# Performance work log

Hardware: AMD Instinct MI355X
Metric: run time of the kernel (lower is better)

## Reference

```python
import jax, jax.numpy as jnp
import numpy as np

N, E, G = 30000, 480000, 64
IN, MID, HEADS, OUT = 256, (64, 64, 128), 8, 13


def _tconv(x, src, dst, ea, qw, qb, kw, kb, vw, vb, ew, sw, sb, heads, n):
    # PyG TransformerConv (concat=True, root_weight=True, beta=False), eval mode
    d = qw.shape[1] // heads
    q = (x @ qw + qb)[dst].reshape(-1, heads, d)   # [E,H,d] query at target
    k = (x @ kw + kb)[src].reshape(-1, heads, d)   # [E,H,d] key at source
    v = (x @ vw + vb)[src].reshape(-1, heads, d)   # [E,H,d] value at source
    e = (ea @ ew).reshape(-1, heads, d)            # [E,H,d] edge embedding (no bias)
    k = k + e
    a = (q * k).sum(-1) / jnp.sqrt(jnp.asarray(d, x.dtype))   # [E,H]
    amax = jax.ops.segment_max(a, dst, num_segments=n)        # segment softmax over in-edges
    ex = jnp.exp(a - amax[dst])
    den = jax.ops.segment_sum(ex, dst, num_segments=n)
    alpha = ex / den[dst]
    out = jax.ops.segment_sum((v + e) * alpha[..., None], dst, num_segments=n)
    out = out.reshape(n, heads * d)
    return out + x @ sw + sb                        # root/skip connection


def _mk(key, shape):
    return jax.random.normal(key, shape, dtype=jnp.float32) * 0.05


def setup_inputs() -> dict:
    key = jax.random.key(0)
    ks = iter(jax.random.split(key, 40))
    inp = {
        "x": jax.random.normal(next(ks), (N, IN), dtype=jnp.float32),
        "edge_index": jax.random.randint(next(ks), (2, E), 0, N, dtype=jnp.int64),
        "edge_attr": jax.random.normal(next(ks), (E, 1), dtype=jnp.float32),
        "batch": jnp.sort(jax.random.randint(next(ks), (N,), 0, G, dtype=jnp.int64)),
    }
    # conv1: in=256 -> heads=8, d=64 (out 512)
    o1 = HEADS * MID[0]
    inp.update(q1w=_mk(next(ks), (IN, o1)), q1b=_mk(next(ks), (o1,)),
               k1w=_mk(next(ks), (IN, o1)), k1b=_mk(next(ks), (o1,)),
               v1w=_mk(next(ks), (IN, o1)), v1b=_mk(next(ks), (o1,)),
               e1w=_mk(next(ks), (1, o1)),
               s1w=_mk(next(ks), (IN, o1)), s1b=_mk(next(ks), (o1,)))
    # conv2: in=512 -> heads=4, d=64 (out 256)
    h2, i2 = HEADS // 2, o1
    o2 = h2 * MID[1]
    inp.update(q2w=_mk(next(ks), (i2, o2)), q2b=_mk(next(ks), (o2,)),
               k2w=_mk(next(ks), (i2, o2)), k2b=_mk(next(ks), (o2,)),
               v2w=_mk(next(ks), (i2, o2)), v2b=_mk(next(ks), (o2,)),
               e2w=_mk(next(ks), (1, o2)),
               s2w=_mk(next(ks), (i2, o2)), s2b=_mk(next(ks), (o2,)))
    # conv3: in=256 -> heads=1, d=128
    i3, o3 = o2, MID[2]
    inp.update(q3w=_mk(next(ks), (i3, o3)), q3b=_mk(next(ks), (o3,)),
               k3w=_mk(next(ks), (i3, o3)), k3b=_mk(next(ks), (o3,)),
               v3w=_mk(next(ks), (i3, o3)), v3b=_mk(next(ks), (o3,)),
               e3w=_mk(next(ks), (1, o3)),
               s3w=_mk(next(ks), (i3, o3)), s3b=_mk(next(ks), (o3,)))
    inp.update(lw=_mk(next(ks), (MID[2], OUT)), lb=_mk(next(ks), (OUT,)))
    return inp


def reference(x, edge_index, edge_attr, batch,
              q1w, q1b, k1w, k1b, v1w, v1b, e1w, s1w, s1b,
              q2w, q2b, k2w, k2b, v2w, v2b, e2w, s2w, s2b,
              q3w, q3b, k3w, k3b, v3w, v3b, e3w, s3w, s3b,
              lw, lb):
    src, dst = edge_index[0], edge_index[1]
    h = _tconv(x, src, dst, edge_attr, q1w, q1b, k1w, k1b, v1w, v1b, e1w, s1w, s1b, HEADS, N)
    h = jax.nn.relu(h)
    h = _tconv(h, src, dst, edge_attr, q2w, q2b, k2w, k2b, v2w, v2b, e2w, s2w, s2b, HEADS // 2, N)
    h = jax.nn.relu(h)
    h = _tconv(h, src, dst, edge_attr, q3w, q3b, k3w, k3b, v3w, v3b, e3w, s3w, s3b, 1, N)
    # global mean pool over graphs
    s = jax.ops.segment_sum(h, batch, num_segments=G)
    cnt = jax.ops.segment_sum(jnp.ones((N,), h.dtype), batch, num_segments=G)
    pooled = s / jnp.maximum(cnt, 1.0)[:, None]
    return pooled @ lw + lb
```

## Files before the change

kernel.cpp:

```cpp
#include <hip/hip_runtime.h>
#include <hip/hip_bf16.h>
#include <cstdint>

#define NN 30000
#define EE 480000
#define GG 64

typedef __attribute__((ext_vector_type(8))) short bf16x8;
typedef __attribute__((ext_vector_type(4))) float float4v;
typedef __attribute__((ext_vector_type(4))) unsigned short ushort4v;

static __device__ inline unsigned short f2bf(float f) {
    unsigned u = __float_as_uint(f);
    unsigned r = (u + 0x7fff + ((u >> 16) & 1)) >> 16;
    return (unsigned short)r;
}
static __device__ inline float bf2f(unsigned short u) {
    return __uint_as_float(((unsigned)u) << 16);
}

__global__ void count_deg_k(const int* __restrict__ ei, int* __restrict__ deg) {
    int e = blockIdx.x * 256 + threadIdx.x;
    if (e < EE) atomicAdd(&deg[ei[EE + e]], 1);
}

__global__ __launch_bounds__(1024) void scan_excl_k(const int* __restrict__ deg,
                                                    int* __restrict__ basep) {
    constexpr int CH = (NN + 1024) / 1024 + 1;
    __shared__ int buf[1024];
    int t = threadIdx.x;
    int b0 = t * CH;
    int loc[CH];
    int s = 0;
#pragma unroll
    for (int i = 0; i < CH; i++) {
        int idx = b0 + i;
        int v = (idx < NN) ? deg[idx] : 0;
        loc[i] = s;
        s += v;
    }
    buf[t] = s;
    __syncthreads();
    for (int off = 1; off < 1024; off <<= 1) {
        int tv = (t >= off) ? buf[t - off] : 0;
        __syncthreads();
        buf[t] += tv;
        __syncthreads();
    }
    int base = (t > 0) ? buf[t - 1] : 0;
#pragma unroll
    for (int i = 0; i < CH; i++) {
        int idx = b0 + i;
        if (idx <= NN) basep[idx] = base + loc[i];
    }
}

__global__ void fill_csr_k(const int* __restrict__ ei, const float* __restrict__ ea,
                           const int* __restrict__ basep, int* __restrict__ cnt,
                           int* __restrict__ csrc, float* __restrict__ cea) {
    int e = blockIdx.x * 256 + threadIdx.x;
    if (e < EE) {
        int d = ei[EE + e];
        int pos = basep[d] + atomicAdd(&cnt[d], 1);
        csrc[pos] = ei[e];
        cea[pos] = ea[e];
    }
}

__global__ void gbound_k(const int* __restrict__ batch, int* __restrict__ gstart) {
    int i = blockIdx.x * 256 + threadIdx.x;
    if (i >= NN) return;
    int cur = batch[i];
    if (i == 0) {
        for (int g = 0; g <= cur; ++g) gstart[g] = 0;
    } else {
        int prev = batch[i - 1];
        for (int g = prev + 1; g <= cur; ++g) gstart[g] = i;
    }
    if (i == NN - 1) {
        for (int g = cur + 1; g <= GG; ++g) gstart[g] = NN;
    }
}

struct PrepDesc { const float* src; void* dst; int rows; int cols; int blk0; int mode; };
#define NDESC 25
struct PrepArgs { PrepDesc d[NDESC]; };

__global__ __launch_bounds__(256) void prep_k(PrepArgs args) {
    int b = blockIdx.x;
    PrepDesc dd = args.d[0];
#pragma unroll
    for (int i = 1; i < NDESC; i++)
        if (b >= args.d[i].blk0) dd = args.d[i];
    int rel = b - dd.blk0;
    int total = dd.rows * dd.cols;
    int base = rel * 1024 + threadIdx.x;
    if (dd.mode == 0) {
        unsigned short* dst = (unsigned short*)dd.dst;
        for (int j = 0; j < 4; j++) {
            int i = base + j * 256;
            if (i < total) dst[i] = f2bf(dd.src[i]);
        }
    } else if (dd.mode == 1) {
        unsigned short* dst = (unsigned short*)dd.dst;
        for (int j = 0; j < 4; j++) {
            int i = base + j * 256;
            if (i < total) {
                int n = i / dd.rows, k = i - n * dd.rows;
                dst[i] = f2bf(dd.src[(size_t)k * dd.cols + n]);
            }
        }
    } else {
        float* dst = (float*)dd.dst;
        for (int j = 0; j < 4; j++) {
            int i = base + j * 256;
            if (i < total) dst[i] = dd.src[i];
        }
    }
}

__global__ __launch_bounds__(256) void gemm_bf16_k(
    const unsigned short* __restrict__ A, const unsigned short* __restrict__ Wt,
    const float* __restrict__ bias, unsigned short* __restrict__ C,
    int M, int K, int N) {
    __shared__ unsigned short As[2][4096];
    __shared__ unsigned short Bs[2][4096];
    int tid = threadIdx.x;
    int lane = tid & 63, wid = tid >> 6;
    int wm = wid >> 1, wn = wid & 1;

    int gx = gridDim.x;
    int T = gx * gridDim.y;
    int lid = blockIdx.y * gx + blockIdx.x;
    int qq = T >> 3, rr = T & 7;
    int xcd = lid & 7, pos = lid >> 3;
    int tile = ((xcd < rr) ? xcd * (qq + 1) : rr * (qq + 1) + (xcd - rr) * qq) + pos;
    int by = tile / gx, bx = tile - by * gx;
    int row0 = by * 128, n0 = bx * 128;

    float4v acc[4][4];
#pragma unroll
    for (int i = 0; i < 4; i++)
#pragma unroll
        for (int j = 0; j < 4; j++) acc[i][j] = (float4v)0.f;

    auto stage = [&](int buf, int k0) {
#pragma unroll
        for (int i = 0; i < 2; ++i) {
            int chunkbase = i * 256 + wid * 64;
            int chunk = chunkbase + lane;
            int r = chunk & 127, kc = chunk >> 7;
            int rowA = row0 + r; if (rowA >= M) rowA = M - 1;
            const unsigned short* ga = A + (size_t)rowA * K + (k0 + kc * 8);
            __builtin_amdgcn_global_load_lds(
                (const __attribute__((address_space(1))) void*)ga,
                (__attribute__((address_space(3))) void*)(As[buf] + (size_t)chunkbase * 8),
                16, 0, 0);
            const unsigned short* gb = Wt + (size_t)(n0 + r) * K + (k0 + kc * 8);
            __builtin_amdgcn_global_load_lds(
                (const __attribute__((address_space(1))) void*)gb,
                (__attribute__((address_space(3))) void*)(Bs[buf] + (size_t)chunkbase * 8),
                16, 0, 0);
        }
    };

    stage(0, 0);
    asm volatile("s_waitcnt vmcnt(0)" ::: "memory");
    __syncthreads();

    int NT = K >> 5;
    for (int t = 0; t < NT; ++t) {
        int b = t & 1;
        if (t + 1 < NT) stage(b ^ 1, (t + 1) << 5);
        bf16x8 af[4], bfr[4];
#pragma unroll
        for (int mi = 0; mi < 4; mi++)
            af[mi] = *(const bf16x8*)(As[b] + ((lane >> 4) * 128 + wm * 64 + mi * 16 + (lane & 15)) * 8);
#pragma unroll
        for (int ni = 0; ni < 4; ni++)
            bfr[ni] = *(const bf16x8*)(Bs[b] + ((lane >> 4) * 128 + wn * 64 + ni * 16 + (lane & 15)) * 8);
#pragma unroll
        for (int mi = 0; mi < 4; mi++)
#pragma unroll
            for (int ni = 0; ni < 4; ni++)
                acc[mi][ni] = __builtin_amdgcn_mfma_f32_16x16x32_bf16(
                    bfr[ni], af[mi], acc[mi][ni], 0, 0, 0);
        asm volatile("s_waitcnt vmcnt(0)" ::: "memory");
        __syncthreads();
    }

    float4v bias4[4];
#pragma unroll
    for (int ni = 0; ni < 4; ni++)
        bias4[ni] = *(const float4v*)&bias[n0 + wn * 64 + ni * 16 + (lane >> 4) * 4];
#pragma unroll
    for (int mi = 0; mi < 4; mi++) {
        int row = row0 + wm * 64 + mi * 16 + (lane & 15);
        if (row < M) {
#pragma unroll
            for (int ni = 0; ni < 4; ni++) {
                int colb = n0 + wn * 64 + ni * 16 + (lane >> 4) * 4;
                ushort4v pk;
#pragma unroll
                for (int r = 0; r < 4; r++) pk[r] = f2bf(acc[mi][ni][r] + bias4[ni][r]);
                *(ushort4v*)(C + (size_t)row * N + colb) = pk;
            }
        }
    }
}

template <int VEC> struct RawVec;
template <> struct RawVec<2> { using T = unsigned; };
template <> struct RawVec<4> { using T = uint2; };
template <> struct RawVec<8> { using T = uint4; };

static __device__ inline void unpackr(unsigned v, float (&r)[2]) {
    r[0] = __uint_as_float(v << 16); r[1] = __uint_as_float(v & 0xffff0000u);
}
static __device__ inline void unpackr(uint2 v, float (&r)[4]) {
    r[0] = __uint_as_float(v.x << 16); r[1] = __uint_as_float(v.x & 0xffff0000u);
    r[2] = __uint_as_float(v.y << 16); r[3] = __uint_as_float(v.y & 0xffff0000u);
}
static __device__ inline void unpackr(uint4 v, float (&r)[8]) {
    r[0] = __uint_as_float(v.x << 16); r[1] = __uint_as_float(v.x & 0xffff0000u);
    r[2] = __uint_as_float(v.y << 16); r[3] = __uint_as_float(v.y & 0xffff0000u);
    r[4] = __uint_as_float(v.z << 16); r[5] = __uint_as_float(v.z & 0xffff0000u);
    r[6] = __uint_as_float(v.w << 16); r[7] = __uint_as_float(v.w & 0xffff0000u);
}

template <int VEC>
__device__ inline void loadbf(const unsigned short* __restrict__ p, float (&r)[VEC]) {
    typename RawVec<VEC>::T v = *(const typename RawVec<VEC>::T*)p;
    unpackr(v, r);
}
template <int VEC>
__device__ inline void loadf32(const float* __restrict__ p, float (&r)[VEC]) {
    if constexpr (VEC == 2) {
        float2 t = *reinterpret_cast<const float2*>(p);
        r[0] = t.x; r[1] = t.y;
    } else {
#pragma unroll
        for (int i = 0; i < VEC; i += 4) {
            float4 t = *reinterpret_cast<const float4*>(p + i);
            r[i] = t.x; r[i + 1] = t.y; r[i + 2] = t.z; r[i + 3] = t.w;
        }
    }
}
template <int VEC>
__device__ inline void storebf(unsigned short* __restrict__ p, const float (&r)[VEC]) {
    unsigned w[VEC / 2];
#pragma unroll
    for (int i = 0; i < VEC / 2; i++)
        w[i] = (unsigned)f2bf(r[2 * i]) | ((unsigned)f2bf(r[2 * i + 1]) << 16);
    if constexpr (VEC == 2) *(unsigned*)p = w[0];
    else if constexpr (VEC == 4) *(uint2*)p = make_uint2(w[0], w[1]);
    else *(uint4*)p = make_uint4(w[0], w[1], w[2], w[3]);
}

template <int H, int D, bool RELU>
__global__ __launch_bounds__(256) void aggregate_k(
    const unsigned short* __restrict__ QKVS, int SR,
    const float* __restrict__ ew,
    const int* __restrict__ rowptr, const int* __restrict__ csrc,
    const float* __restrict__ cea, unsigned short* __restrict__ Hout) {
    constexpr int F = H * D;
    constexpr int VEC = F / 64;
    constexpr int L = 64 / H;
    using RawT = typename RawVec<VEC>::T;
    int lane = threadIdx.x & 63;
    int node = blockIdx.x * 4 + (threadIdx.x >> 6);
    if (node >= NN) return;

    const unsigned short* qrow = QKVS + (size_t)node * SR;
    float q[VEC], ewv[VEC], acc[VEC];
    loadbf<VEC>(qrow + lane * VEC, q);
    loadf32<VEC>(ew + lane * VEC, ewv);
#pragma unroll
    for (int i = 0; i < VEC; i++) acc[i] = 0.f;

    float den = 0.f;
    const float isd = rsqrtf((float)D);
    int beg = rowptr[node], end = rowptr[node + 1];

    for (int cb = beg; cb < end; cb += 64) {
        int cnt = min(end - cb, 64);
        int gi = cb + lane;
        int sidx = (gi < end) ? csrc[gi] : 0;
        float sea = (gi < end) ? cea[gi] : 0.f;

        RawT k0r, k1r, k2r, k3r, v0r, v1r, v2r, v3r;
        float e0 = 0.f, e1 = 0.f, e2 = 0.f, e3 = 0.f;
        auto fetch = [&](int t, RawT& kr, RawT& vr, float& ea) {
            int s = __shfl(sidx, t, 64);
            ea = __shfl(sea, t, 64);
            const unsigned short* b = QKVS + (size_t)s * SR + F + lane * VEC;
            kr = *(const RawT*)b;
            vr = *(const RawT*)(b + F);
        };
        auto process = [&](RawT kr, RawT vr, float ea) {
            float kv[VEC], vv[VEC], t[VEC];
            unpackr(kr, kv);
            unpackr(vr, vv);
            float p = 0.f;
#pragma unroll
            for (int i = 0; i < VEC; i++) { t[i] = ea * ewv[i]; p += q[i] * (kv[i] + t[i]); }
#pragma unroll
            for (int off = 1; off < L; off <<= 1) p += __shfl_xor(p, off, 64);
            float w = __expf(fminf(p * isd, 30.f));
            den += w;
#pragma unroll
            for (int i = 0; i < VEC; i++) acc[i] += w * (vv[i] + t[i]);
        };

        if (cnt > 0) fetch(0, k0r, v0r, e0);
        if (cnt > 1) fetch(1, k1r, v1r, e1);
        if (cnt > 2) fetch(2, k2r, v2r, e2);
        if (cnt > 3) fetch(3, k3r, v3r, e3);

        for (int t = 0; t < cnt; t += 4) {
            process(k0r, v0r, e0);
            if (t + 4 < cnt) fetch(t + 4, k0r, v0r, e0);
            if (t + 1 < cnt) {
                process(k1r, v1r, e1);
                if (t + 5 < cnt) fetch(t + 5, k1r, v1r, e1);
            }
            if (t + 2 < cnt) {
                process(k2r, v2r, e2);
                if (t + 6 < cnt) fetch(t + 6, k2r, v2r, e2);
            }
            if (t + 3 < cnt) {
                process(k3r, v3r, e3);
                if (t + 7 < cnt) fetch(t + 7, k3r, v3r, e3);
            }
        }
    }

    float rden = (den > 0.f) ? 1.f / den : 0.f;
    float sv[VEC];
    loadbf<VEC>(qrow + 3 * F + lane * VEC, sv);
    float o[VEC];
#pragma unroll
    for (int i = 0; i < VEC; i++) {
        float v = acc[i] * rden + sv[i];
        o[i] = RELU ? fmaxf(v, 0.f) : v;
    }
    storebf<VEC>(Hout + (size_t)node * F + lane * VEC, o);
}

__global__ __launch_bounds__(256) void pool_head_k(
    const unsigned short* __restrict__ h3, const int* __restrict__ gstart,
    const float* __restrict__ lw, const float* __restrict__ lb,
    float* __restrict__ out) {
    __shared__ float part[256];
    __shared__ float pooled[128];
    int g = blockIdx.x;
    int beg = gstart[g], end = gstart[g + 1];
    int d = threadIdx.x & 127, half = threadIdx.x >> 7;
    float s = 0.f;
    for (int node = beg + half; node < end; node += 2)
        s += bf2f(h3[(size_t)node * 128 + d]);
    part[threadIdx.x] = s;
    __syncthreads();
    if (threadIdx.x < 128) {
        float cnt = fmaxf((float)(end - beg), 1.0f);
        pooled[threadIdx.x] = (part[threadIdx.x] + part[threadIdx.x + 128]) / cnt;
    }
    __syncthreads();
    if (threadIdx.x < 13) {
        float acc = lb[threadIdx.x];
        for (int dd = 0; dd < 128; ++dd)
            acc += pooled[dd] * lw[dd * 13 + threadIdx.x];
        out[g * 13 + threadIdx.x] = acc;
    }
}

__global__ void ws_fail_k(float* __restrict__ out, int n) {
    int i = blockIdx.x * 256 + threadIdx.x;
    if (i < n) out[i] = -12345.0f;
}

extern "C" void kernel_launch(void* const* d_in, const int* in_sizes, int n_in,
                              void* d_out, int out_size, void* d_ws, size_t ws_size,
                              hipStream_t stream) {
    const float* x   = (const float*)d_in[0];
    const int*   ei  = (const int*)d_in[1];
    const float* ea  = (const float*)d_in[2];
    const int*   bat = (const int*)d_in[3];
    const float* W1[4] = {(const float*)d_in[4], (const float*)d_in[6], (const float*)d_in[8], (const float*)d_in[11]};
    const float* B1[4] = {(const float*)d_in[5], (const float*)d_in[7], (const float*)d_in[9], (const float*)d_in[12]};
    const float* e1w = (const float*)d_in[10];
    const float* W2[4] = {(const float*)d_in[13], (const float*)d_in[15], (const float*)d_in[17], (const float*)d_in[20]};
    const float* B2[4] = {(const float*)d_in[14], (const float*)d_in[16], (const float*)d_in[18], (const float*)d_in[21]};
    const float* e2w = (const float*)d_in[19];
    const float* W3[4] = {(const float*)d_in[22], (const float*)d_in[24], (const float*)d_in[26], (const float*)d_in[29]};
    const float* B3[4] = {(const float*)d_in[23], (const float*)d_in[25], (const float*)d_in[27], (const float*)d_in[30]};
    const float* e3w = (const float*)d_in[28];
    const float* lw  = (const float*)d_in[31];
    const float* lb  = (const float*)d_in[32];

    char* wsb = (char*)d_ws;
    size_t off = 0;
    auto alloc_b = [&](size_t bytes) {
        void* p = wsb + off;
        off += (bytes + 255) & ~(size_t)255;
        return p;
    };
    unsigned short* xb   = (unsigned short*)alloc_b((size_t)NN * 256 * 2);
    unsigned short* Wc1  = (unsigned short*)alloc_b((size_t)2048 * 256 * 2);
    float*          bc1  = (float*)alloc_b(2048 * 4);
    unsigned short* Wc2  = (unsigned short*)alloc_b((size_t)1024 * 512 * 2);
    float*          bc2  = (float*)alloc_b(1024 * 4);
    unsigned short* Wc3  = (unsigned short*)alloc_b((size_t)512 * 256 * 2);
    float*          bc3  = (float*)alloc_b(512 * 4);
    unsigned short* QKVS = (unsigned short*)alloc_b((size_t)NN * 2048 * 2);
    unsigned short* H1   = (unsigned short*)alloc_b((size_t)NN * 512 * 2);
    unsigned short* H2   = (unsigned short*)alloc_b((size_t)NN * 256 * 2);
    unsigned short* H3   = (unsigned short*)alloc_b((size_t)NN * 128 * 2);
    int*   basep  = (int*)alloc_b((NN + 1) * 4);
    int*   csrc   = (int*)alloc_b((size_t)EE * 4);
    float* cea    = (float*)alloc_b((size_t)EE * 4);
    int*   gstart = (int*)alloc_b((GG + 1) * 4);
    size_t zstart = off;
    int*   deg    = (int*)alloc_b(NN * 4);
    int*   cnt    = (int*)alloc_b(NN * 4);
    size_t zbytes = off - zstart;

    if (ws_size < off) {
        ws_fail_k<<<(out_size + 255) / 256, 256, 0, stream>>>((float*)d_out, out_size);
        return;
    }

    hipMemsetAsync(wsb + zstart, 0, zbytes, stream);

    PrepArgs pa;
    int blk = 0, di = 0;
    auto add = [&](const float* src, void* dst, int rows, int cols, int mode) {
        pa.d[di].src = src; pa.d[di].dst = dst;
        pa.d[di].rows = rows; pa.d[di].cols = cols;
        pa.d[di].mode = mode; pa.d[di].blk0 = blk;
        blk += (rows * cols + 1023) / 1024;
        di++;
    };
    add(x, xb, NN * 256, 1, 0);
    for (int s = 0; s < 4; s++) add(W1[s], Wc1 + (size_t)s * 512 * 256, 256, 512, 1);
    for (int s = 0; s < 4; s++) add(B1[s], bc1 + s * 512, 512, 1, 2);
    for (int s = 0; s < 4; s++) add(W2[s], Wc2 + (size_t)s * 256 * 512, 512, 256, 1);
    for (int s = 0; s < 4; s++) add(B2[s], bc2 + s * 256, 256, 1, 2);
    for (int s = 0; s < 4; s++) add(W3[s], Wc3 + (size_t)s * 128 * 256, 256, 128, 1);
    for (int s = 0; s < 4; s++) add(B3[s], bc3 + s * 128, 128, 1, 2);
    prep_k<<<blk, 256, 0, stream>>>(pa);

    int eblocks = (EE + 255) / 256;
    count_deg_k<<<eblocks, 256, 0, stream>>>(ei, deg);
    scan_excl_k<<<1, 1024, 0, stream>>>(deg, basep);
    fill_csr_k<<<eblocks, 256, 0, stream>>>(ei, ea, basep, cnt, csrc, cea);
    gbound_k<<<(NN + 255) / 256, 256, 0, stream>>>(bat, gstart);

    int mblocks = (NN + 127) / 128;
    gemm_bf16_k<<<dim3(2048 / 128, mblocks), 256, 0, stream>>>(xb, Wc1, bc1, QKVS, NN, 256, 2048);
    aggregate_k<8, 64, true><<<NN / 4, 256, 0, stream>>>(QKVS, 2048, e1w, basep, csrc, cea, H1);
    gemm_bf16_k<<<dim3(1024 / 128, mblocks), 256, 0, stream>>>(H1, Wc2, bc2, QKVS, NN, 512, 1024);
    aggregate_k<4, 64, true><<<NN / 4, 256, 0, stream>>>(QKVS, 1024, e2w, basep, csrc, cea, H2);
    gemm_bf16_k<<<dim3(512 / 128, mblocks), 256, 0, stream>>>(H2, Wc3, bc3, QKVS, NN, 256, 512);
    aggregate_k<1, 128, false><<<NN / 4, 256, 0, stream>>>(QKVS, 512, e3w, basep, csrc, cea, H3);

    pool_head_k<<<GG, 256, 0, stream>>>(H3, gstart, lw, lb, (float*)d_out);
}
```

Before: 775.0 us.

## Split each node's edge loop across two wavefronts and merge via shared memory

The aggregation kernel now assigns two wavefronts per destination node, each handling alternating in-edges (even/odd), with prefetch depth kept at four per wave. Partial softmax denominators and accumulators from the odd wave are written to LDS and summed by the even wave after a block barrier. This doubles the memory-level parallelism per node to hide gather latency, at the cost of twice as many blocks, a __syncthreads, and LDS traffic.

```diff
diff --git a/kernel.cpp b/kernel.cpp
--- a/kernel.cpp
+++ b/kernel.cpp
@@ -267,9 +267,14 @@
     constexpr int VEC = F / 64;
     constexpr int L = 64 / H;
     using RawT = typename RawVec<VEC>::T;
+    __shared__ float accbuf[2][F];
+    __shared__ float denbuf[2][64];
+
     int lane = threadIdx.x & 63;
-    int node = blockIdx.x * 4 + (threadIdx.x >> 6);
-    if (node >= NN) return;
+    int wid = threadIdx.x >> 6;
+    int nl = wid >> 1;
+    int parity = wid & 1;
+    int node = blockIdx.x * 2 + nl;
 
     const unsigned short* qrow = QKVS + (size_t)node * SR;
     float q[VEC], ewv[VEC], acc[VEC];
@@ -290,9 +295,9 @@
 
         RawT k0r, k1r, k2r, k3r, v0r, v1r, v2r, v3r;
         float e0 = 0.f, e1 = 0.f, e2 = 0.f, e3 = 0.f;
-        auto fetch = [&](int t, RawT& kr, RawT& vr, float& ea) {
-            int s = __shfl(sidx, t, 64);
-            ea = __shfl(sea, t, 64);
+        auto fetch = [&](int p, RawT& kr, RawT& vr, float& ea) {
+            int s = __shfl(sidx, p, 64);
+            ea = __shfl(sea, p, 64);
             const unsigned short* b = QKVS + (size_t)s * SR + F + lane * VEC;
             kr = *(const RawT*)b;
             vr = *(const RawT*)(b + F);
@@ -312,39 +317,51 @@
             for (int i = 0; i < VEC; i++) acc[i] += w * (vv[i] + t[i]);
         };
 
-        if (cnt > 0) fetch(0, k0r, v0r, e0);
-        if (cnt > 1) fetch(1, k1r, v1r, e1);
-        if (cnt > 2) fetch(2, k2r, v2r, e2);
-        if (cnt > 3) fetch(3, k3r, v3r, e3);
-
-        for (int t = 0; t < cnt; t += 4) {
+        if (parity + 0 < cnt) fetch(parity + 0, k0r, v0r, e0);
+        if (parity + 2 < cnt) fetch(parity + 2, k1r, v1r, e1);
+        if (parity + 4 < cnt) fetch(parity + 4, k2r, v2r, e2);
+        if (parity + 6 < cnt) fetch(parity + 6, k3r, v3r, e3);
+
+        for (int u = parity; u < cnt; u += 8) {
             process(k0r, v0r, e0);
-            if (t + 4 < cnt) fetch(t + 4, k0r, v0r, e0);
-            if (t + 1 < cnt) {
+            if (u + 8 < cnt) fetch(u + 8, k0r, v0r, e0);
+            if (u + 2 < cnt) {
                 process(k1r, v1r, e1);
-                if (t + 5 < cnt) fetch(t + 5, k1r, v1r, e1);
+                if (u + 10 < cnt) fetch(u + 10, k1r, v1r, e1);
             }
-            if (t + 2 < cnt) {
+            if (u + 4 < cnt) {
                 process(k2r, v2r, e2);
-                if (t + 6 < cnt) fetch(t + 6, k2r, v2r, e2);
+                if (u + 12 < cnt) fetch(u + 12, k2r, v2r, e2);
             }
-            if (t + 3 < cnt) {
+            if (u + 6 < cnt) {
                 process(k3r, v3r, e3);
-                if (t + 7 < cnt) fetch(t + 7, k3r, v3r, e3);
+                if (u + 14 < cnt) fetch(u + 14, k3r, v3r, e3);
             }
         }
     }
 
-    float rden = (den > 0.f) ? 1.f / den : 0.f;
-    float sv[VEC];
-    loadbf<VEC>(qrow + 3 * F + lane * VEC, sv);
-    float o[VEC];
-#pragma unroll
-    for (int i = 0; i < VEC; i++) {
-        float v = acc[i] * rden + sv[i];
-        o[i] = RELU ? fmaxf(v, 0.f) : v;
-    }
-    storebf<VEC>(Hout + (size_t)node * F + lane * VEC, o);
+    if (parity == 1) {
+        denbuf[nl][lane] = den;
+#pragma unroll
+        for (int i = 0; i < VEC; i++) accbuf[nl][lane * VEC + i] = acc[i];
+    }
+    __syncthreads();
+    if (parity == 0) {
+        den += denbuf[nl][lane];
+#pragma unroll
+        for (int i = 0; i < VEC; i++) acc[i] += accbuf[nl][lane * VEC + i];
+
+        float rden = (den > 0.f) ? 1.f / den : 0.f;
+        float sv[VEC];
+        loadbf<VEC>(qrow + 3 * F + lane * VEC, sv);
+        float o[VEC];
+#pragma unroll
+        for (int i = 0; i < VEC; i++) {
+            float v = acc[i] * rden + sv[i];
+            o[i] = RELU ? fmaxf(v, 0.f) : v;
+        }
+        storebf<VEC>(Hout + (size_t)node * F + lane * VEC, o);
+    }
 }
 
 __global__ __launch_bounds__(256) void pool_head_k(
@@ -458,11 +475,11 @@
 
     int mblocks = (NN + 127) / 128;
     gemm_bf16_k<<<dim3(2048 / 128, mblocks), 256, 0, stream>>>(xb, Wc1, bc1, QKVS, NN, 256, 2048);
-    aggregate_k<8, 64, true><<<NN / 4, 256, 0, stream>>>(QKVS, 2048, e1w, basep, csrc, cea, H1);
+    aggregate_k<8, 64, true><<<NN / 2, 256, 0, stream>>>(QKVS, 2048, e1w, basep, csrc, cea, H1);
     gemm_bf16_k<<<dim3(1024 / 128, mblocks), 256, 0, stream>>>(H1, Wc2, bc2, QKVS, NN, 512, 1024);
-    aggregate_k<4, 64, true><<<NN / 4, 256, 0, stream>>>(QKVS, 1024, e2w, basep, csrc, cea, H2);
+    aggregate_k<4, 64, true><<<NN / 2, 256, 0, stream>>>(QKVS, 1024, e2w, basep, csrc, cea, H2);
     gemm_bf16_k<<<dim3(512 / 128, mblocks), 256, 0, stream>>>(H2, Wc3, bc3, QKVS, NN, 256, 512);
-    aggregate_k<1, 128, false><<<NN / 4, 256, 0, stream>>>(QKVS, 512, e3w, basep, csrc, cea, H3);
+    aggregate_k<1, 128, false><<<NN / 2, 256, 0, stream>>>(QKVS, 512, e3w, basep, csrc, cea, H3);
 
     pool_head_k<<<GG, 256, 0, stream>>>(H3, gstart, lw, lb, (float*)d_out);
 }
```

After: 775.8 us. About the same (+0.1%).
